# Kernel optimization log

Measured on AMD Instinct MI355X. Metric: run time of the kernel, lower is better.

Reference implementation:

```python
import jax, jax.numpy as jnp
import numpy as np

W_IMG = 512
H_IMG = 512
D_MODEL = 192
N_FREQ = 8
LN_EPS = 1e-5


def _fourier_pe(coords_norm):
    # coords_norm: [B,K,2] in [0,1); returns [B,K,4*N_FREQ]
    freqs = 2.0 ** jnp.arange(N_FREQ, dtype=jnp.float32)  # [F]
    two_pi = 2.0 * jnp.pi
    x = coords_norm[..., 0:1] * freqs * two_pi  # [B,K,F]
    y = coords_norm[..., 1:2] * freqs * two_pi
    return jnp.concatenate([jnp.sin(x), jnp.cos(x), jnp.sin(y), jnp.cos(y)], axis=-1)


def _bilinear_sample(feat, gx, gy):
    # feat: [B,C,H,W]; gx,gy: [B,K] normalized coords in [-1,1], align_corners=True
    B, C, H, W = feat.shape
    ix = (gx + 1.0) * 0.5 * (W - 1)
    iy = (gy + 1.0) * 0.5 * (H - 1)
    ix0 = jnp.floor(ix)
    iy0 = jnp.floor(iy)
    wx = ix - ix0  # [B,K]
    wy = iy - iy0
    x0 = jnp.clip(ix0.astype(jnp.int32), 0, W - 1)
    x1 = jnp.clip(ix0.astype(jnp.int32) + 1, 0, W - 1)
    y0 = jnp.clip(iy0.astype(jnp.int32), 0, H - 1)
    y1 = jnp.clip(iy0.astype(jnp.int32) + 1, 0, H - 1)
    b = jnp.arange(B)[:, None]  # [B,1] broadcast against [B,K]
    g = lambda y, x: feat[b, :, y, x]  # [B,K,C]
    out = (g(y0, x0) * ((1 - wx) * (1 - wy))[..., None]
           + g(y0, x1) * (wx * (1 - wy))[..., None]
           + g(y1, x0) * ((1 - wx) * wy)[..., None]
           + g(y1, x1) * (wx * wy)[..., None])
    return out  # [B,K,C]


def setup_inputs() -> dict:
    key = jax.random.key(0)
    ks = jax.random.split(key, 16)
    B, K = 8, 4096
    # pixel coordinates in [0, W_IMG-1] x [0, H_IMG-1]
    u = jax.random.uniform(ks[0], (B, K, 2), dtype=jnp.float32)
    coords = u * jnp.array([W_IMG - 1, H_IMG - 1], dtype=jnp.float32)
    L1 = jax.random.normal(ks[1], (B, D_MODEL, 128, 128), dtype=jnp.float32)
    L2 = jax.random.normal(ks[2], (B, D_MODEL, 64, 64), dtype=jnp.float32)
    L3 = jax.random.normal(ks[3], (B, D_MODEL, 32, 32), dtype=jnp.float32)
    L4 = jax.random.normal(ks[4], (B, D_MODEL, 16, 16), dtype=jnp.float32)
    d_in = D_MODEL * 4 + 4 * N_FREQ  # 800
    Wseed_w = jax.random.normal(ks[5], (D_MODEL, d_in), dtype=jnp.float32) / np.sqrt(d_in)
    Wseed_b = jnp.zeros((D_MODEL,), dtype=jnp.float32)
    ln_g = jnp.ones((D_MODEL,), dtype=jnp.float32)
    ln_b = jnp.zeros((D_MODEL,), dtype=jnp.float32)
    Wpos_w = jax.random.normal(ks[6], (D_MODEL, 4 * N_FREQ), dtype=jnp.float32) / np.sqrt(4 * N_FREQ)
    Wpos_b = jnp.zeros((D_MODEL,), dtype=jnp.float32)
    return {"coords": coords, "L1": L1, "L2": L2, "L3": L3, "L4": L4,
            "Wseed_w": Wseed_w, "Wseed_b": Wseed_b, "ln_g": ln_g, "ln_b": ln_b,
            "Wpos_w": Wpos_w, "Wpos_b": Wpos_b}


def reference(coords, L1, L2, L3, L4, Wseed_w, Wseed_b, ln_g, ln_b, Wpos_w, Wpos_b):
    B, K, _ = coords.shape
    # normalized grid in [-1,1] (x uses W, y uses H), align_corners=True convention
    gx = 2.0 * coords[..., 0] / (W_IMG - 1) - 1.0  # [B,K]
    gy = 2.0 * coords[..., 1] / (H_IMG - 1) - 1.0
    center_grid = jnp.stack([gx, gy], axis=-1).reshape(B, K, 1, 2)
    coords_norm = coords / jnp.array([W_IMG, H_IMG], dtype=jnp.float32)
    pe_q = _fourier_pe(coords_norm)  # [B,K,32]
    f1 = _bilinear_sample(L1, gx, gy)
    f2 = _bilinear_sample(L2, gx, gy)
    f3 = _bilinear_sample(L3, gx, gy)
    f4 = _bilinear_sample(L4, gx, gy)
    x = jnp.concatenate([f1, f2, f3, f4, pe_q], axis=-1)  # [B,K,800]
    seed = x @ Wseed_w.T + Wseed_b
    mu = jnp.mean(seed, axis=-1, keepdims=True)
    var = jnp.mean((seed - mu) ** 2, axis=-1, keepdims=True)
    seed = (seed - mu) / jnp.sqrt(var + LN_EPS) * ln_g + ln_b
    pos = pe_q @ Wpos_w.T + Wpos_b
    return (seed, pos, center_grid)
```

## Files before the change

kernel.cpp:

```cpp
#include <hip/hip_runtime.h>
#include <hip/hip_bf16.h>
#include <stdint.h>

typedef unsigned short u16;
typedef short s16x8 __attribute__((ext_vector_type(8)));
typedef float f32x4 __attribute__((ext_vector_type(4)));
typedef uint32_t u32x4 __attribute__((ext_vector_type(4)));

typedef const __attribute__((address_space(1))) void* gas_t;
typedef __attribute__((address_space(3))) void* las_t;

__device__ __forceinline__ uint32_t pack_bf16(float lo, float hi) {
  float2 f; f.x = lo; f.y = hi;
  __hip_bfloat162 h = __float22bfloat162_rn(f);
  union { __hip_bfloat162 h; uint32_t u; } c; c.h = h;
  return c.u;
}
__device__ __forceinline__ u16 f2bf(float f) {
  union { float f; uint32_t u; } a; a.f = f;
  uint32_t u = a.u;
  return (u16)((u + 0x7fffu + ((u >> 16) & 1u)) >> 16);
}
__device__ __forceinline__ float bf2f(uint32_t hbits) {
  union { uint32_t u; float f; } a; a.u = hbits << 16;
  return a.f;
}

__device__ __forceinline__ u32x4 bilin4(u32x4 q00, u32x4 q01, u32x4 q10, u32x4 q11,
                                        float w00, float w01, float w10, float w11) {
  u32x4 o;
#pragma unroll
  for (int k = 0; k < 4; ++k) {
    float lo = bf2f(q00[k] & 0xffff) * w00 + bf2f(q01[k] & 0xffff) * w01 +
               bf2f(q10[k] & 0xffff) * w10 + bf2f(q11[k] & 0xffff) * w11;
    float hi = bf2f(q00[k] >> 16) * w00 + bf2f(q01[k] >> 16) * w01 +
               bf2f(q10[k] >> 16) * w10 + bf2f(q11[k] >> 16) * w11;
    o[k] = pack_bf16(lo, hi);
  }
  return o;
}

__global__ __launch_bounds__(512, 6) void prep_all(
    const float* __restrict__ L1, const float* __restrict__ L2,
    const float* __restrict__ L3, const float* __restrict__ L4,
    const float* __restrict__ ws_w, const float* __restrict__ wp_w,
    u16* __restrict__ T1, u16* __restrict__ T2,
    u16* __restrict__ T3, u16* __restrict__ T4,
    u16* __restrict__ dWs, u16* __restrict__ dWp) {
  const int bid = blockIdx.x;
  const int t = threadIdx.x;

  if (bid >= 2720) {
    int t0 = (bid - 2720) * 512 + t;
    for (int i = t0; i < 39936; i += 16384) {
      if (i < 38400) {
        int e4 = 4 * i;
        int n = e4 / 800;
        int k = e4 - n * 800;
        f32x4 v = *(const f32x4*)(ws_w + e4);
        int nt = n >> 4, mrow = n & 15;
        int kc = k >> 5, quad = (k >> 3) & 3, e0 = k & 7;
        int dst = ((nt * 25 + kc) * 64 + (quad * 16 + mrow)) * 8 + e0;
        uint2 o;
        o.x = pack_bf16(v.x, v.y);
        o.y = pack_bf16(v.z, v.w);
        *(uint2*)(dWs + dst) = o;
      } else {
        int j = i - 38400;
        int e4 = 4 * j;
        int n = e4 >> 5, k = e4 & 31;
        f32x4 v = *(const f32x4*)(wp_w + e4);
        int nt = n >> 4, mrow = n & 15;
        int quad = k >> 3, e0 = k & 7;
        int dst = (nt * 64 + (quad * 16 + mrow)) * 8 + e0;
        uint2 o;
        o.x = pack_bf16(v.x, v.y);
        o.y = pack_bf16(v.z, v.w);
        *(uint2*)(dWp + dst) = o;
      }
    }
    return;
  }

  const float* src; u16* dst; int HW, tpl, rel;
  if (bid < 2048)      { src = L1; dst = T1; HW = 16384; tpl = 256; rel = bid; }
  else if (bid < 2560) { src = L2; dst = T2; HW = 4096;  tpl = 64;  rel = bid - 2048; }
  else if (bid < 2688) { src = L3; dst = T3; HW = 1024;  tpl = 16;  rel = bid - 2560; }
  else                 { src = L4; dst = T4; HW = 256;   tpl = 4;   rel = bid - 2688; }
  const int b = rel / tpl, r = rel % tpl;
  const int hw0 = (r >> 1) * 128;
  const int c0 = (r & 1) * 96;

  __shared__ __align__(16) float tileF[96 * 128];
  const float* sb = src + (size_t)b * 192 * HW + (size_t)c0 * HW + hw0;

  const int l = t & 63, w = t >> 6;
#pragma unroll
  for (int i = 0; i < 6; ++i) {
    int k = w * 6 + i;
    int c = 2 * k + (l >> 5);
    int q = c >> 3;
    int hwf = ((l & 31) << 2) ^ ((q & 7) << 2);
    __builtin_amdgcn_global_load_lds(
        (gas_t)(sb + (size_t)c * HW + hwf),
        (las_t)(tileF + k * 256),
        16, 0, 0);
  }
  __syncthreads();

  uint32_t* d = (uint32_t*)(dst + ((size_t)b * HW + hw0) * 192) + (c0 >> 1);
#pragma unroll
  for (int i = 0; i < 3; ++i) {
    int e = i * 512 + t;
    int hw = e / 12, q = e - hw * 12;
    const float* rp = tileF + (q * 8) * 128 + (hw ^ ((q & 7) << 2));
    u32x4 v;
#pragma unroll
    for (int j = 0; j < 4; ++j)
      v[j] = pack_bf16(rp[(2 * j) * 128], rp[(2 * j + 1) * 128]);
    *(u32x4*)(d + hw * 96 + q * 4) = v;
  }
}

__global__ __launch_bounds__(256, 6) void seed_main(
    const float* __restrict__ coords,
    const u16* __restrict__ T1, const u16* __restrict__ T2,
    const u16* __restrict__ T3, const u16* __restrict__ T4,
    const u16* __restrict__ Wseed, const u16* __restrict__ Wpos,
    const float* __restrict__ seed_b, const float* __restrict__ ln_g,
    const float* __restrict__ ln_b, const float* __restrict__ pos_b,
    float* __restrict__ out_seed, float* __restrict__ out_pos,
    float* __restrict__ out_cg) {

  __shared__ __align__(16) u16 xt[16 * 808];
  __shared__ float mu_s[16], rs_s[16];

  const int t = threadIdx.x;
  const int gp0 = blockIdx.x * 16;
  const int b = gp0 >> 12;

  if (t < 32) {
    int p = t >> 1, xy = t & 1;
    float c = coords[(gp0 + p) * 2 + xy];
    out_cg[(gp0 + p) * 2 + xy] = c * (2.0f / 511.0f) - 1.0f;
  }
  for (int i = 0; i < 2; ++i) {
    int e = i * 256 + t;
    int p = e >> 5, j = e & 31;
    float c = coords[(gp0 + p) * 2 + ((j >> 4) & 1)] * (1.0f / 512.0f);
    float v = c * (float)(1 << (j & 7));
    float a = (v - floorf(v)) * 6.283185307179586f;
    float r = (j & 8) ? __cosf(a) : __sinf(a);
    xt[p * 808 + 768 + j] = f2bf(r);
  }

  {
    const u16* B1 = T1 + (size_t)b * 16384 * 192;
    const u16* B2 = T2 + (size_t)b * 4096 * 192;
    const u16* B3 = T3 + (size_t)b * 1024 * 192;
    const u16* B4 = T4 + (size_t)b * 256 * 192;
    int plv = t >> 2;
    int lv = plv & 3, p = plv >> 2;
    int c4b = t & 3;
    float cx = coords[(gp0 + p) * 2 + 0];
    float cy = coords[(gp0 + p) * 2 + 1];
    float gx = cx * (2.0f / 511.0f) - 1.0f;
    float gy = cy * (2.0f / 511.0f) - 1.0f;
    int Wl = 128 >> lv;
    float ix = (gx + 1.0f) * 0.5f * (float)(Wl - 1);
    float iy = (gy + 1.0f) * 0.5f * (float)(Wl - 1);
    float fx = floorf(ix), fy = floorf(iy);
    float wx = ix - fx, wy = iy - fy;
    int x0 = (int)fx, y0 = (int)fy;
    int x1 = min(max(x0 + 1, 0), Wl - 1), y1 = min(max(y0 + 1, 0), Wl - 1);
    x0 = min(max(x0, 0), Wl - 1); y0 = min(max(y0, 0), Wl - 1);
    const u16* base = (lv == 0) ? B1 : (lv == 1) ? B2 : (lv == 2) ? B3 : B4;
    const u16* b00 = base + (y0 * Wl + x0) * 192;
    const u16* b01 = base + (y0 * Wl + x1) * 192;
    const u16* b10 = base + (y1 * Wl + x0) * 192;
    const u16* b11 = base + (y1 * Wl + x1) * 192;
    float w00 = (1.0f - wx) * (1.0f - wy), w01 = wx * (1.0f - wy);
    float w10 = (1.0f - wx) * wy,          w11 = wx * wy;
    u16* dstp = xt + p * 808 + lv * 192;
    int cph = (c4b + lv) & 3;
    int cc = cph * 8;
    u32x4 q00 = *(const u32x4*)(b00 + cc);
    u32x4 q01 = *(const u32x4*)(b01 + cc);
    u32x4 q10 = *(const u32x4*)(b10 + cc);
    u32x4 q11 = *(const u32x4*)(b11 + cc);
#pragma unroll
    for (int i = 0; i < 5; ++i) {
      int cn = cc + 32;
      u32x4 n00 = *(const u32x4*)(b00 + cn);
      u32x4 n01 = *(const u32x4*)(b01 + cn);
      u32x4 n10 = *(const u32x4*)(b10 + cn);
      u32x4 n11 = *(const u32x4*)(b11 + cn);
      *(u32x4*)(dstp + cc) = bilin4(q00, q01, q10, q11, w00, w01, w10, w11);
      cc = cn;
      q00 = n00; q01 = n01; q10 = n10; q11 = n11;
    }
    *(u32x4*)(dstp + cc) = bilin4(q00, q01, q10, q11, w00, w01, w10, w11);
  }
  __syncthreads();

  const int lid = t & 63, wv = t >> 6;
  const int quad = lid >> 4, mrow = lid & 15;
  const int nt0 = wv * 3;

  f32x4 accS[3];
#pragma unroll
  for (int j = 0; j < 3; ++j) accS[j] = (f32x4)0.0f;

  const u16* ws = Wseed + (size_t)nt0 * 12800 + lid * 8;
  const u16* arow = xt + mrow * 808 + quad * 8;

  s16x8 a  = *(const s16x8*)(arow);
  s16x8 b0 = *(const s16x8*)(ws);
  s16x8 b1 = *(const s16x8*)(ws + 12800);
  s16x8 b2 = *(const s16x8*)(ws + 25600);
#pragma unroll 6
  for (int kc = 0; kc < 24; ++kc) {
    s16x8 an = *(const s16x8*)(arow + (kc + 1) * 32);
    const u16* wp = ws + (kc + 1) * 512;
    s16x8 b0n = *(const s16x8*)(wp);
    s16x8 b1n = *(const s16x8*)(wp + 12800);
    s16x8 b2n = *(const s16x8*)(wp + 25600);
    accS[0] = __builtin_amdgcn_mfma_f32_16x16x32_bf16(a, b0, accS[0], 0, 0, 0);
    accS[1] = __builtin_amdgcn_mfma_f32_16x16x32_bf16(a, b1, accS[1], 0, 0, 0);
    accS[2] = __builtin_amdgcn_mfma_f32_16x16x32_bf16(a, b2, accS[2], 0, 0, 0);
    a = an; b0 = b0n; b1 = b1n; b2 = b2n;
  }
  accS[0] = __builtin_amdgcn_mfma_f32_16x16x32_bf16(a, b0, accS[0], 0, 0, 0);
  accS[1] = __builtin_amdgcn_mfma_f32_16x16x32_bf16(a, b1, accS[1], 0, 0, 0);
  accS[2] = __builtin_amdgcn_mfma_f32_16x16x32_bf16(a, b2, accS[2], 0, 0, 0);

#pragma unroll
  for (int j = 0; j < 3; ++j) {
    s16x8 bw = *(const s16x8*)(Wpos + (size_t)(nt0 + j) * 512 + lid * 8);
    f32x4 ap = (f32x4)0.0f;
    ap = __builtin_amdgcn_mfma_f32_16x16x32_bf16(a, bw, ap, 0, 0, 0);
    int n = (nt0 + j) * 16 + mrow;
    float pb = pos_b[n];
#pragma unroll
    for (int r = 0; r < 4; ++r)
      out_pos[(size_t)(gp0 + quad * 4 + r) * 192 + n] = ap[r] + pb;
  }

  __syncthreads();
  float* preLN = (float*)xt;
#pragma unroll
  for (int j = 0; j < 3; ++j) {
    int n = (nt0 + j) * 16 + mrow;
    float sb = seed_b[n];
#pragma unroll
    for (int r = 0; r < 4; ++r)
      preLN[(quad * 4 + r) * 193 + n] = accS[j][r] + sb;
  }
  __syncthreads();

  {
    int r = t >> 4, g = t & 15;
    float s = 0.0f, sq = 0.0f;
#pragma unroll
    for (int i = 0; i < 12; ++i) {
      float v = preLN[r * 193 + g * 12 + i];
      s += v; sq += v * v;
    }
#pragma unroll
    for (int d = 8; d > 0; d >>= 1) {
      s += __shfl_down(s, d, 16);
      sq += __shfl_down(sq, d, 16);
    }
    if (g == 0) {
      float mu = s * (1.0f / 192.0f);
      float var = sq * (1.0f / 192.0f) - mu * mu;
      mu_s[r] = mu;
      rs_s[r] = 1.0f / sqrtf(var + 1e-5f);
    }
  }
  __syncthreads();

  for (int i = 0; i < 12; ++i) {
    int e = i * 256 + t;
    int r = e / 192, n = e - r * 192;
    float v = (preLN[r * 193 + n] - mu_s[r]) * rs_s[r] * ln_g[n] + ln_b[n];
    out_seed[(size_t)(gp0 + r) * 192 + n] = v;
  }
}

extern "C" void kernel_launch(void* const* d_in, const int* in_sizes, int n_in,
                              void* d_out, int out_size, void* d_ws, size_t ws_size,
                              hipStream_t stream) {
  const float* coords  = (const float*)d_in[0];
  const float* L1      = (const float*)d_in[1];
  const float* L2      = (const float*)d_in[2];
  const float* L3      = (const float*)d_in[3];
  const float* L4      = (const float*)d_in[4];
  const float* Wseed_w = (const float*)d_in[5];
  const float* Wseed_b = (const float*)d_in[6];
  const float* ln_g    = (const float*)d_in[7];
  const float* ln_b    = (const float*)d_in[8];
  const float* Wpos_w  = (const float*)d_in[9];
  const float* Wpos_b  = (const float*)d_in[10];

  u16* T1  = (u16*)d_ws;
  u16* T2  = T1 + (size_t)8 * 16384 * 192;
  u16* T3  = T2 + (size_t)8 * 4096 * 192;
  u16* T4  = T3 + (size_t)8 * 1024 * 192;
  u16* Wsd = T4 + (size_t)8 * 256 * 192;
  u16* Wps = Wsd + 153600;

  prep_all<<<2752, 512, 0, stream>>>(L1, L2, L3, L4, Wseed_w, Wpos_w,
                                     T1, T2, T3, T4, Wsd, Wps);

  float* out_seed = (float*)d_out;
  float* out_pos  = out_seed + (size_t)32768 * 192;
  float* out_cg   = out_pos  + (size_t)32768 * 192;

  seed_main<<<2048, 256, 0, stream>>>(coords, T1, T2, T3, T4, Wsd, Wps,
                                      Wseed_b, ln_g, ln_b, Wpos_b,
                                      out_seed, out_pos, out_cg);
}
```

Before: 259.3 us.

## Make prep_all persistent with double-buffered LDS transpose pipeline

The feature-map transpose/bf16 conversion kernel changes from one block per 96x128 tile to 768 persistent blocks. Each block walks several jobs split into 48-channel halves and double-buffers the async global-to-LDS loads, so the next load overlaps the current store. This removes the per-block launch and drain serialization and the single-shot load-then-store stall. In exchange it adds manual waitcnt and barrier management and narrower 8-byte stores. There is also a harmless self-assignment typo on out_pos.

```diff
diff --git a/kernel.cpp b/kernel.cpp
--- a/kernel.cpp
+++ b/kernel.cpp
@@ -50,8 +50,8 @@
   const int bid = blockIdx.x;
   const int t = threadIdx.x;
 
-  if (bid >= 2720) {
-    int t0 = (bid - 2720) * 512 + t;
+  if (bid >= 768) {
+    int t0 = (bid - 768) * 512 + t;
     for (int i = t0; i < 39936; i += 16384) {
       if (i < 38400) {
         int e4 = 4 * i;
@@ -82,43 +82,77 @@
     return;
   }
 
-  const float* src; u16* dst; int HW, tpl, rel;
-  if (bid < 2048)      { src = L1; dst = T1; HW = 16384; tpl = 256; rel = bid; }
-  else if (bid < 2560) { src = L2; dst = T2; HW = 4096;  tpl = 64;  rel = bid - 2048; }
-  else if (bid < 2688) { src = L3; dst = T3; HW = 1024;  tpl = 16;  rel = bid - 2560; }
-  else                 { src = L4; dst = T4; HW = 256;   tpl = 4;   rel = bid - 2688; }
-  const int b = rel / tpl, r = rel % tpl;
-  const int hw0 = (r >> 1) * 128;
-  const int c0 = (r & 1) * 96;
-
-  __shared__ __align__(16) float tileF[96 * 128];
-  const float* sb = src + (size_t)b * 192 * HW + (size_t)c0 * HW + hw0;
+  __shared__ __align__(16) float bufs[2][48 * 128];
 
   const int l = t & 63, w = t >> 6;
-#pragma unroll
-  for (int i = 0; i < 6; ++i) {
-    int k = w * 6 + i;
-    int c = 2 * k + (l >> 5);
-    int q = c >> 3;
-    int hwf = ((l & 31) << 2) ^ ((q & 7) << 2);
-    __builtin_amdgcn_global_load_lds(
-        (gas_t)(sb + (size_t)c * HW + hwf),
-        (las_t)(tileF + k * 256),
-        16, 0, 0);
-  }
-  __syncthreads();
-
-  uint32_t* d = (uint32_t*)(dst + ((size_t)b * HW + hw0) * 192) + (c0 >> 1);
-#pragma unroll
-  for (int i = 0; i < 3; ++i) {
-    int e = i * 512 + t;
-    int hw = e / 12, q = e - hw * 12;
-    const float* rp = tileF + (q * 8) * 128 + (hw ^ ((q & 7) << 2));
-    u32x4 v;
-#pragma unroll
-    for (int j = 0; j < 4; ++j)
-      v[j] = pack_bf16(rp[(2 * j) * 128], rp[(2 * j + 1) * 128]);
-    *(u32x4*)(d + hw * 96 + q * 4) = v;
+  const int nsub = ((bid < 416) ? 4 : 3) * 2;
+
+  auto issue = [&](int m, float* buf) {
+    int job = bid + (m >> 1) * 768;
+    int s = m & 1;
+    const float* src; int HW, tpl, rel;
+    if (job < 2048)      { src = L1; HW = 16384; tpl = 256; rel = job; }
+    else if (job < 2560) { src = L2; HW = 4096;  tpl = 64;  rel = job - 2048; }
+    else if (job < 2688) { src = L3; HW = 1024;  tpl = 16;  rel = job - 2560; }
+    else                 { src = L4; HW = 256;   tpl = 4;   rel = job - 2688; }
+    int b = rel / tpl, r = rel % tpl;
+    int hw0 = (r >> 1) * 128;
+    int c0 = (r & 1) * 96 + 48 * s;
+    const float* sb = src + ((size_t)b * 192 + c0) * HW + hw0;
+#pragma unroll
+    for (int i = 0; i < 3; ++i) {
+      int k = w * 3 + i;
+      int crel = 2 * k + (l >> 5);
+      int hwf = ((l & 31) << 2) ^ (((crel >> 3) & 7) << 2);
+      __builtin_amdgcn_global_load_lds(
+          (gas_t)(sb + (size_t)crel * HW + hwf),
+          (las_t)(buf + k * 256),
+          16, 0, 0);
+    }
+  };
+
+  auto store = [&](int m, const float* buf) {
+    int job = bid + (m >> 1) * 768;
+    int s = m & 1;
+    u16* dst; int HW, tpl, rel;
+    if (job < 2048)      { dst = T1; HW = 16384; tpl = 256; rel = job; }
+    else if (job < 2560) { dst = T2; HW = 4096;  tpl = 64;  rel = job - 2048; }
+    else if (job < 2688) { dst = T3; HW = 1024;  tpl = 16;  rel = job - 2560; }
+    else                 { dst = T4; HW = 256;   tpl = 4;   rel = job - 2688; }
+    int b = rel / tpl, r = rel % tpl;
+    int hw0 = (r >> 1) * 128;
+    int c0 = (r & 1) * 96 + 48 * s;
+    uint32_t* d = (uint32_t*)(dst + ((size_t)b * HW + hw0) * 192) + (c0 >> 1);
+#pragma unroll
+    for (int i = 0; i < 3; ++i) {
+      int e = i * 512 + t;
+      int hw = e / 12, q2 = e - hw * 12;
+      float f0 = buf[(q2 * 4 + 0) * 128 + (hw ^ (((q2 * 4 + 0) >> 3) << 2))];
+      float f1 = buf[(q2 * 4 + 1) * 128 + (hw ^ (((q2 * 4 + 1) >> 3) << 2))];
+      float f2 = buf[(q2 * 4 + 2) * 128 + (hw ^ (((q2 * 4 + 2) >> 3) << 2))];
+      float f3 = buf[(q2 * 4 + 3) * 128 + (hw ^ (((q2 * 4 + 3) >> 3) << 2))];
+      uint2 v;
+      v.x = pack_bf16(f0, f1);
+      v.y = pack_bf16(f2, f3);
+      *(uint2*)(d + hw * 96 + q2 * 2) = v;
+    }
+  };
+
+  issue(0, bufs[0]);
+  int cur = 0;
+  for (int m = 0; m < nsub; ++m) {
+    if (m + 1 < nsub) {
+      issue(m + 1, bufs[cur ^ 1]);
+      asm volatile("s_waitcnt vmcnt(3)" ::: "memory");
+    } else {
+      asm volatile("s_waitcnt vmcnt(0)" ::: "memory");
+    }
+    __builtin_amdgcn_s_barrier();
+    __builtin_amdgcn_sched_barrier(0);
+    store(m, bufs[cur]);
+    __builtin_amdgcn_s_barrier();
+    __builtin_amdgcn_sched_barrier(0);
+    cur ^= 1;
   }
 }
 
@@ -310,11 +344,11 @@
   u16* Wsd = T4 + (size_t)8 * 256 * 192;
   u16* Wps = Wsd + 153600;
 
-  prep_all<<<2752, 512, 0, stream>>>(L1, L2, L3, L4, Wseed_w, Wpos_w,
-                                     T1, T2, T3, T4, Wsd, Wps);
+  prep_all<<<800, 512, 0, stream>>>(L1, L2, L3, L4, Wseed_w, Wpos_w,
+                                    T1, T2, T3, T4, Wsd, Wps);
 
   float* out_seed = (float*)d_out;
-  float* out_pos  = out_seed + (size_t)32768 * 192;
+  float* out_pos  = out_pos = out_seed + (size_t)32768 * 192;
   float* out_cg   = out_pos  + (size_t)32768 * 192;
 
   seed_main<<<2048, 256, 0, stream>>>(coords, T1, T2, T3, T4, Wsd, Wps,
```

Result: slower. 267.9 us (+3.3%).
